# Optimization experiments

Measured on AMD Instinct MI355X. Metric: run time of the kernel, lower is better.

Reference implementation:

```python
import jax, jax.numpy as jnp
import numpy as np

N, D, K = 500_000, 64, 512


def setup_inputs() -> dict:
    key = jax.random.key(0)
    kx, kc = jax.random.split(key)
    x = jax.random.normal(kx, (N, D), dtype=jnp.float32)
    centroids = jax.random.normal(kc, (K, D), dtype=jnp.float32)
    return {"x": x, "centroids": centroids}


def reference(x, centroids):
    x2 = jnp.sum(x * x, axis=1, keepdims=True)            # [N, 1]
    c2 = jnp.sum(centroids * centroids, axis=1)           # [K]
    d2 = x2 + c2[None, :] - 2.0 * jnp.einsum('nd,kd->nk', x, centroids)
    d2 = jnp.maximum(d2, 0.0)
    # sqrt is monotonic so argmin over d2 == argmin over cdist
    label = jnp.argmin(d2, axis=1)                        # [N] int
    return label
```

## Files before the change

### kernel.cpp

```cpp
#include <hip/hip_runtime.h>

#define DIM 64
#define KC 512
#define BLK 256
#define BLKP 256
#define RSB 256
#define PT 2
#define CG 32
#define NT (CG / 16)
#define NGRP (KC / CG)
#define MARGINH 5e-4f
#define LIST_CAP 500000

typedef _Float16 half8   __attribute__((ext_vector_type(8)));
typedef float    floatx4 __attribute__((ext_vector_type(4)));

__device__ __forceinline__ void async_cp16(_Float16* lds_base, const _Float16* g_lane) {
    __builtin_amdgcn_global_load_lds(
        (const __attribute__((address_space(1))) unsigned int*)(g_lane),
        (__attribute__((address_space(3))) unsigned int*)(lds_base),
        16, 0, 0);
}

__global__ __launch_bounds__(BLKP) void kmeans_prep(
    const float* __restrict__ c, _Float16* __restrict__ frH,
    _Float16* __restrict__ frL, float* __restrict__ g_sc2,
    float* __restrict__ g_negh, unsigned* __restrict__ rs_count)
{
    const int b = blockIdx.x;
    if (b < 128) {
        const int e  = b * BLKP + threadIdx.x;
        const int cr = e >> 6, d = e & 63;
        const int T  = cr >> 4, ni = cr & 15;
        const int ch = d >> 5, q = (d >> 3) & 3, j = d & 7;
        const int pos = ((T * 2 + ch) * 64 + (q * 16 + ni)) * 8 + j;
        const float f = c[e];
        const _Float16 h = (_Float16)f;
        frH[pos] = h;
        frL[pos] = (_Float16)((f - (float)h) * 2048.0f);
    } else {
        if (b == 128 && threadIdx.x == 0) *rs_count = 0u;
        const int k = (b - 128) * BLKP + threadIdx.x;
        const float* crow = c + (long)k * DIM;
        float s0 = 0.f, s1 = 0.f, s2 = 0.f, s3 = 0.f;
        #pragma unroll
        for (int d = 0; d < DIM; d += 4) {
            s0 = fmaf(crow[d + 0], crow[d + 0], s0);
            s1 = fmaf(crow[d + 1], crow[d + 1], s1);
            s2 = fmaf(crow[d + 2], crow[d + 2], s2);
            s3 = fmaf(crow[d + 3], crow[d + 3], s3);
        }
        const float s = (s0 + s1) + (s2 + s3);
        g_sc2[k]  = s;
        g_negh[k] = -0.5f * s;
    }
}

__global__ __launch_bounds__(BLK)
__attribute__((amdgpu_waves_per_eu(2)))
void kmeans_mfma(const float* __restrict__ x,
                 const _Float16* __restrict__ frH, const _Float16* __restrict__ frL,
                 const float* __restrict__ g_negh, int* __restrict__ out,
                 unsigned* __restrict__ rs_count, int* __restrict__ rs_list, int n)
{
    __shared__ _Float16 shH[2][NT * 2 * 64 * 8];
    __shared__ _Float16 shL[2][NT * 2 * 64 * 8];
    __shared__ float    s_negh[KC];

    const int tid  = threadIdx.x;
    const int wave = tid >> 6;
    const int lane = tid & 63;
    const int nidx = lane & 15;
    const int quad = lane >> 4;

    const long jobBase = ((long)blockIdx.x * 4 + wave) * (PT * 16);

    auto stage = [&](int gg, int buf) {
        const _Float16* srcH = frH + (long)gg * (NT * 2 * 64 * 8);
        const _Float16* srcL = frL + (long)gg * (NT * 2 * 64 * 8);
        const int chunk = wave * 64;
        async_cp16(&shH[buf][(long)chunk * 8], srcH + (long)(chunk + lane) * 8);
        async_cp16(&shL[buf][(long)chunk * 8], srcL + (long)(chunk + lane) * 8);
    };

    stage(0, 0);
    for (int k2 = tid; k2 < KC; k2 += BLK) s_negh[k2] = g_negh[k2];

    half8 ah[PT][2], al[PT][2];
    #pragma unroll
    for (int pt = 0; pt < PT; ++pt) {
        long row = jobBase + pt * 16 + nidx;
        if (row > (long)n - 1) row = (long)n - 1;
        #pragma unroll
        for (int ch = 0; ch < 2; ++ch) {
            const float* xp = x + row * DIM + ch * 32 + quad * 8;
            float4 v0 = *(const float4*)xp;
            float4 v1 = *(const float4*)(xp + 4);
            float fs[8] = {v0.x, v0.y, v0.z, v0.w, v1.x, v1.y, v1.z, v1.w};
            #pragma unroll
            for (int j = 0; j < 8; ++j) {
                _Float16 h = (_Float16)fs[j];
                ah[pt][ch][j] = h;
                al[pt][ch][j] = (_Float16)((fs[j] - (float)h) * 2048.0f);
            }
        }
    }

    float best[PT][4], sec[PT][4];
    int   bidx[PT][4];
    #pragma unroll
    for (int pt = 0; pt < PT; ++pt)
        #pragma unroll
        for (int r = 0; r < 4; ++r) {
            best[pt][r] = -3.402823466e38f;
            sec[pt][r]  = -3.402823466e38f;
            bidx[pt][r] = 0;
        }

    const floatx4 ZERO = {0.f, 0.f, 0.f, 0.f};

    __syncthreads();

    for (int g = 0; g < NGRP; ++g) {
        const int cur = g & 1;
        if (g + 1 < NGRP) stage(g + 1, cur ^ 1);

        #pragma unroll
        for (int t = 0; t < NT; ++t) {
            const half8 bh0 = *(const half8*)&shH[cur][((t * 2 + 0) * 64 + lane) * 8];
            const half8 bh1 = *(const half8*)&shH[cur][((t * 2 + 1) * 64 + lane) * 8];
            const half8 bl0 = *(const half8*)&shL[cur][((t * 2 + 0) * 64 + lane) * 8];
            const half8 bl1 = *(const half8*)&shL[cur][((t * 2 + 1) * 64 + lane) * 8];
            const int   kidx  = g * CG + t * 16 + nidx;
            const float ng    = s_negh[kidx];
            const floatx4 cinit = {ng, ng, ng, ng};
            #pragma unroll
            for (int pt = 0; pt < PT; ++pt) {
                floatx4 am, ac;
                am = __builtin_amdgcn_mfma_f32_16x16x32_f16(ah[pt][0], bh0, cinit, 0, 0, 0);
                am = __builtin_amdgcn_mfma_f32_16x16x32_f16(ah[pt][1], bh1, am, 0, 0, 0);
                ac = __builtin_amdgcn_mfma_f32_16x16x32_f16(ah[pt][0], bl0, ZERO, 0, 0, 0);
                ac = __builtin_amdgcn_mfma_f32_16x16x32_f16(ah[pt][1], bl1, ac, 0, 0, 0);
                ac = __builtin_amdgcn_mfma_f32_16x16x32_f16(al[pt][0], bh0, ac, 0, 0, 0);
                ac = __builtin_amdgcn_mfma_f32_16x16x32_f16(al[pt][1], bh1, ac, 0, 0, 0);
                const floatx4 vv = am + ac * 4.8828125e-4f;
                #pragma unroll
                for (int r = 0; r < 4; ++r) {
                    const bool gt = vv[r] > best[pt][r];
                    sec[pt][r]  = __builtin_amdgcn_fmed3f(sec[pt][r], vv[r], best[pt][r]);
                    best[pt][r] = fmaxf(best[pt][r], vv[r]);
                    bidx[pt][r] = gt ? kidx : bidx[pt][r];
                }
            }
        }
        if (g + 1 < NGRP) __syncthreads();
    }

    #pragma unroll
    for (int off = 1; off < 16; off <<= 1) {
        #pragma unroll
        for (int pt = 0; pt < PT; ++pt)
            #pragma unroll
            for (int r = 0; r < 4; ++r) {
                const float ob = __shfl_xor(best[pt][r], off, 64);
                const int   oi = __shfl_xor(bidx[pt][r], off, 64);
                const float os = __shfl_xor(sec[pt][r],  off, 64);
                const bool take = (ob > best[pt][r]) ||
                                  (ob == best[pt][r] && oi < bidx[pt][r]);
                const float loser = take ? best[pt][r] : ob;
                sec[pt][r]  = fmaxf(fmaxf(sec[pt][r], os), loser);
                best[pt][r] = take ? ob : best[pt][r];
                bidx[pt][r] = take ? oi : bidx[pt][r];
            }
    }

    const int pt_w = nidx >> 2;
    const int r_w  = nidx & 3;
    float b = 0.f, s = 0.f; int bi = 0;
    #pragma unroll
    for (int pt = 0; pt < PT; ++pt)
        #pragma unroll
        for (int r = 0; r < 4; ++r) {
            const bool m = (pt == pt_w) && (r == r_w);
            b  = m ? best[pt][r] : b;
            s  = m ? sec[pt][r]  : s;
            bi = m ? bidx[pt][r] : bi;
        }
    const long p = jobBase + (long)pt_w * 16 + quad * 4 + r_w;

    const bool valid = (nidx < 8) && (p < n);
    if (valid) out[p] = bi;
    const bool need  = valid && !(b - s > MARGINH);

    const unsigned long long m = __ballot(need);
    if (m) {
        const int leader = (int)(__ffsll((unsigned long long)m) - 1);
        unsigned base = 0;
        if (lane == leader) base = atomicAdd(rs_count, (unsigned)__popcll(m));
        base = __shfl(base, leader, 64);
        if (need) {
            const unsigned idx = base + (unsigned)__popcll(m & ((1ull << lane) - 1ull));
            if (idx < LIST_CAP) rs_list[idx] = (int)p;
        }
    }
}

__global__ __launch_bounds__(RSB) void kmeans_rescan(
    const float* __restrict__ x, const float* __restrict__ c,
    const float* __restrict__ g_sc2, const unsigned* __restrict__ rs_count,
    const int* __restrict__ rs_list, int* __restrict__ out)
{
    __shared__ float4 ct4[16 * 513];
    __shared__ float  s_c2[KC];

    unsigned cnt = *rs_count;
    if (cnt > LIST_CAP) cnt = LIST_CAP;
    if ((unsigned)(blockIdx.x * (RSB / 64)) >= cnt) return;

    const int tid = threadIdx.x;
    for (int e = tid; e < KC * 16; e += RSB) {
        const int k = e >> 4, d4 = e & 15;
        ct4[d4 * 513 + k] = *(const float4*)(c + (long)k * DIM + d4 * 4);
    }
    for (int k = tid; k < KC; k += RSB) s_c2[k] = g_sc2[k];
    __syncthreads();

    const int lane  = tid & 63;
    const int gwave = blockIdx.x * (RSB / 64) + (tid >> 6);
    const int nwave = gridDim.x * (RSB / 64);

    for (unsigned j = gwave; j < cnt; j += nwave) {
        const int p = rs_list[j];
        const float* xrow = x + (long)p * DIM;

        float x20 = 0.f, x21 = 0.f, x22 = 0.f, x23 = 0.f;
        #pragma unroll
        for (int d = 0; d < DIM; d += 4) {
            x20 = fmaf(xrow[d + 0], xrow[d + 0], x20);
            x21 = fmaf(xrow[d + 1], xrow[d + 1], x21);
            x22 = fmaf(xrow[d + 2], xrow[d + 2], x22);
            x23 = fmaf(xrow[d + 3], xrow[d + 3], x23);
        }
        const float x2 = (x20 + x21) + (x22 + x23);

        float bb = 3.402823466e38f; int bbi = 0x7fffffff;
        #pragma unroll
        for (int kk = 0; kk < 8; ++kk) {
            const int k = kk * 64 + lane;
            float d0 = 0.f, d1 = 0.f, d2a = 0.f, d3 = 0.f;
            #pragma unroll
            for (int d4 = 0; d4 < 16; ++d4) {
                const float4 q = ct4[d4 * 513 + k];
                d0  = fmaf(q.x, xrow[4 * d4 + 0], d0);
                d1  = fmaf(q.y, xrow[4 * d4 + 1], d1);
                d2a = fmaf(q.z, xrow[4 * d4 + 2], d2a);
                d3  = fmaf(q.w, xrow[4 * d4 + 3], d3);
            }
            const float dot = (d0 + d1) + (d2a + d3);
            float d2v = (x2 + s_c2[k]) - 2.0f * dot;
            d2v = fmaxf(d2v, 0.0f);
            const bool l2 = (d2v < bb) || (d2v == bb && k < bbi);
            bb  = l2 ? d2v : bb;
            bbi = l2 ? k   : bbi;
        }
        #pragma unroll
        for (int off = 1; off < 64; off <<= 1) {
            const float ob = __shfl_xor(bb, off, 64);
            const int   oi = __shfl_xor(bbi, off, 64);
            const bool take = (ob < bb) || (ob == bb && oi < bbi);
            bb  = take ? ob : bb;
            bbi = take ? oi : bbi;
        }
        if (lane == 0) out[p] = bbi;
    }
}

extern "C" void kernel_launch(void* const* d_in, const int* in_sizes, int n_in,
                              void* d_out, int out_size, void* d_ws, size_t ws_size,
                              hipStream_t stream) {
    const float* x = (const float*)d_in[0];
    const float* c = (const float*)d_in[1];
    int* out = (int*)d_out;
    const int n = in_sizes[0] / DIM;

    _Float16* frH   = (_Float16*)d_ws;
    _Float16* frL   = frH + (KC * DIM);
    float*    gsc2  = (float*)(frL + (KC * DIM));
    float*    gnegh = gsc2 + KC;
    unsigned* cnt   = (unsigned*)(gnegh + KC);
    int*      rlist = (int*)(cnt + 4);

    kmeans_prep<<<130, BLKP, 0, stream>>>(c, frH, frL, gsc2, gnegh, cnt);

    const int jobs   = (n + PT * 16 - 1) / (PT * 16);
    const int blocks = (jobs + 3) / 4;
    kmeans_mfma<<<blocks, BLK, 0, stream>>>(x, frH, frL, gnegh, out, cnt, rlist, n);

    kmeans_rescan<<<256, RSB, 0, stream>>>(x, c, gsc2, cnt, rlist, out);
}
```

Before: 292.9 us.

## Read centroid fragments from global directly and pack tile index into score bits

The staged double-buffered LDS pipeline and its block barriers are removed, and centroid fragments and norms are now loaded straight from global (L1/L2-cached) memory each tile. The per-candidate argmin index tracking is replaced by encoding the tile index in the low 5 mantissa bits of the score. The bias term is folded in through a fused multiply-add before the hi×hi MFMAs, and each wave now handles 3 row tiles instead of 2. The margin is widened to cover the lost mantissa precision, which can send more rows to the rescan pass. Direct global loads may also add latency per tile.

```diff
diff --git a/kernel.cpp b/kernel.cpp
--- a/kernel.cpp
+++ b/kernel.cpp
@@ -5,22 +5,15 @@
 #define BLK 256
 #define BLKP 256
 #define RSB 256
-#define PT 2
-#define CG 32
-#define NT (CG / 16)
-#define NGRP (KC / CG)
-#define MARGINH 5e-4f
+#define PT 3
+#define NTILE (KC / 16)
 #define LIST_CAP 500000
+
+#define MARGINH 2.0e-3f
+#define SCALE_LO 4.8828125e-4f
 
 typedef _Float16 half8   __attribute__((ext_vector_type(8)));
 typedef float    floatx4 __attribute__((ext_vector_type(4)));
-
-__device__ __forceinline__ void async_cp16(_Float16* lds_base, const _Float16* g_lane) {
-    __builtin_amdgcn_global_load_lds(
-        (const __attribute__((address_space(1))) unsigned int*)(g_lane),
-        (__attribute__((address_space(3))) unsigned int*)(lds_base),
-        16, 0, 0);
-}
 
 __global__ __launch_bounds__(BLKP) void kmeans_prep(
     const float* __restrict__ c, _Float16* __restrict__ frH,
@@ -63,10 +56,6 @@
                  const float* __restrict__ g_negh, int* __restrict__ out,
                  unsigned* __restrict__ rs_count, int* __restrict__ rs_list, int n)
 {
-    __shared__ _Float16 shH[2][NT * 2 * 64 * 8];
-    __shared__ _Float16 shL[2][NT * 2 * 64 * 8];
-    __shared__ float    s_negh[KC];
-
     const int tid  = threadIdx.x;
     const int wave = tid >> 6;
     const int lane = tid & 63;
@@ -75,16 +64,8 @@
 
     const long jobBase = ((long)blockIdx.x * 4 + wave) * (PT * 16);
 
-    auto stage = [&](int gg, int buf) {
-        const _Float16* srcH = frH + (long)gg * (NT * 2 * 64 * 8);
-        const _Float16* srcL = frL + (long)gg * (NT * 2 * 64 * 8);
-        const int chunk = wave * 64;
-        async_cp16(&shH[buf][(long)chunk * 8], srcH + (long)(chunk + lane) * 8);
-        async_cp16(&shL[buf][(long)chunk * 8], srcL + (long)(chunk + lane) * 8);
-    };
-
-    stage(0, 0);
-    for (int k2 = tid; k2 < KC; k2 += BLK) s_negh[k2] = g_negh[k2];
+    const half8* __restrict__ gH = (const half8*)frH;
+    const half8* __restrict__ gL = (const half8*)frL;
 
     half8 ah[PT][2], al[PT][2];
     #pragma unroll
@@ -107,54 +88,53 @@
     }
 
     float best[PT][4], sec[PT][4];
-    int   bidx[PT][4];
     #pragma unroll
     for (int pt = 0; pt < PT; ++pt)
         #pragma unroll
         for (int r = 0; r < 4; ++r) {
             best[pt][r] = -3.402823466e38f;
             sec[pt][r]  = -3.402823466e38f;
-            bidx[pt][r] = 0;
         }
 
     const floatx4 ZERO = {0.f, 0.f, 0.f, 0.f};
 
-    __syncthreads();
-
-    for (int g = 0; g < NGRP; ++g) {
-        const int cur = g & 1;
-        if (g + 1 < NGRP) stage(g + 1, cur ^ 1);
-
-        #pragma unroll
-        for (int t = 0; t < NT; ++t) {
-            const half8 bh0 = *(const half8*)&shH[cur][((t * 2 + 0) * 64 + lane) * 8];
-            const half8 bh1 = *(const half8*)&shH[cur][((t * 2 + 1) * 64 + lane) * 8];
-            const half8 bl0 = *(const half8*)&shL[cur][((t * 2 + 0) * 64 + lane) * 8];
-            const half8 bl1 = *(const half8*)&shL[cur][((t * 2 + 1) * 64 + lane) * 8];
-            const int   kidx  = g * CG + t * 16 + nidx;
-            const float ng    = s_negh[kidx];
-            const floatx4 cinit = {ng, ng, ng, ng};
-            #pragma unroll
-            for (int pt = 0; pt < PT; ++pt) {
-                floatx4 am, ac;
-                am = __builtin_amdgcn_mfma_f32_16x16x32_f16(ah[pt][0], bh0, cinit, 0, 0, 0);
-                am = __builtin_amdgcn_mfma_f32_16x16x32_f16(ah[pt][1], bh1, am, 0, 0, 0);
-                ac = __builtin_amdgcn_mfma_f32_16x16x32_f16(ah[pt][0], bl0, ZERO, 0, 0, 0);
-                ac = __builtin_amdgcn_mfma_f32_16x16x32_f16(ah[pt][1], bl1, ac, 0, 0, 0);
-                ac = __builtin_amdgcn_mfma_f32_16x16x32_f16(al[pt][0], bh0, ac, 0, 0, 0);
-                ac = __builtin_amdgcn_mfma_f32_16x16x32_f16(al[pt][1], bh1, ac, 0, 0, 0);
-                const floatx4 vv = am + ac * 4.8828125e-4f;
-                #pragma unroll
-                for (int r = 0; r < 4; ++r) {
-                    const bool gt = vv[r] > best[pt][r];
-                    sec[pt][r]  = __builtin_amdgcn_fmed3f(sec[pt][r], vv[r], best[pt][r]);
-                    best[pt][r] = fmaxf(best[pt][r], vv[r]);
-                    bidx[pt][r] = gt ? kidx : bidx[pt][r];
-                }
-            }
-        }
-        if (g + 1 < NGRP) __syncthreads();
-    }
+    for (int T = 0; T < NTILE; ++T) {
+        const int off = T * 128 + lane;
+        const half8 bh0 = gH[off];
+        const half8 bh1 = gH[off + 64];
+        const half8 bl0 = gL[off];
+        const half8 bl1 = gL[off + 64];
+        const float ng  = g_negh[T * 16 + nidx];
+
+        #pragma unroll
+        for (int pt = 0; pt < PT; ++pt) {
+            floatx4 ac;
+            ac = __builtin_amdgcn_mfma_f32_16x16x32_f16(ah[pt][0], bl0, ZERO, 0, 0, 0);
+            ac = __builtin_amdgcn_mfma_f32_16x16x32_f16(ah[pt][1], bl1, ac, 0, 0, 0);
+            ac = __builtin_amdgcn_mfma_f32_16x16x32_f16(al[pt][0], bh0, ac, 0, 0, 0);
+            ac = __builtin_amdgcn_mfma_f32_16x16x32_f16(al[pt][1], bh1, ac, 0, 0, 0);
+            floatx4 c5;
+            #pragma unroll
+            for (int r = 0; r < 4; ++r) c5[r] = fmaf(ac[r], SCALE_LO, ng);
+            floatx4 vv;
+            vv = __builtin_amdgcn_mfma_f32_16x16x32_f16(ah[pt][0], bh0, c5, 0, 0, 0);
+            vv = __builtin_amdgcn_mfma_f32_16x16x32_f16(ah[pt][1], bh1, vv, 0, 0, 0);
+            #pragma unroll
+            for (int r = 0; r < 4; ++r) {
+                const float vp = __uint_as_float(
+                    (__float_as_uint(vv[r]) & 0xFFFFFFE0u) | (unsigned)T);
+                sec[pt][r]  = __builtin_amdgcn_fmed3f(sec[pt][r], vp, best[pt][r]);
+                best[pt][r] = fmaxf(best[pt][r], vp);
+            }
+        }
+    }
+
+    int bidx[PT][4];
+    #pragma unroll
+    for (int pt = 0; pt < PT; ++pt)
+        #pragma unroll
+        for (int r = 0; r < 4; ++r)
+            bidx[pt][r] = (int)((__float_as_uint(best[pt][r]) & 31u) << 4) + nidx;
 
     #pragma unroll
     for (int off = 1; off < 16; off <<= 1) {
@@ -188,7 +168,7 @@
         }
     const long p = jobBase + (long)pt_w * 16 + quad * 4 + r_w;
 
-    const bool valid = (nidx < 8) && (p < n);
+    const bool valid = (nidx < PT * 4) && (p < n);
     if (valid) out[p] = bi;
     const bool need  = valid && !(b - s > MARGINH);
 
```

New measurement: 309.6 us. 1.06x slower.
